# Optimization experiments

Hardware: AMD Instinct MI355X
Metric: run time of the kernel (lower is better)

Reference implementation:

```python
import jax, jax.numpy as jnp
import numpy as np

D = 768       # input_size
C = 8000      # num_classes
S = 4096      # seq_len
B = 2         # batch
SCALE = 1.0
LN_EPS = 1e-5


def setup_inputs() -> dict:
    key = jax.random.key(0)
    ks = jax.random.split(key, 8)
    std = 0.03  # module's _init_weights std
    return {
        "x": jax.random.normal(ks[0], (B, S, D), dtype=jnp.float32),
        "encoded_descriptions": jax.random.normal(ks[1], (C, D), dtype=jnp.float32),
        "Wk": jax.random.normal(ks[2], (D, D), dtype=jnp.float32) * std,
        "Wv": jax.random.normal(ks[3], (D, D), dtype=jnp.float32) * std,
        "bv": jax.random.normal(ks[4], (D,), dtype=jnp.float32) * 0.01,
        "ln_gamma": jnp.ones((D,), dtype=jnp.float32),
        "ln_beta": jnp.zeros((D,), dtype=jnp.float32),
        "out_w": jax.random.normal(ks[5], (D,), dtype=jnp.float32) * std,
        "out_b": jax.random.normal(ks[6], (), dtype=jnp.float32) * 0.01,
    }


def reference(x, encoded_descriptions, Wk, Wv, bv, ln_gamma, ln_beta, out_w, out_b):
    # V = x @ Wv^T + bv ; K = x @ Wk^T  (torch Linear applies weight transposed)
    V = jnp.einsum('bsd,ed->bse', x, Wv) + bv          # [B, S, D]
    K = jnp.einsum('bsd,ed->bse', x, Wk)               # [B, S, D]
    # att_weights = Q @ K^T, Q broadcast over batch -> [B, C, S]
    att = jnp.einsum('cd,bsd->bcs', encoded_descriptions, K)
    attention = jax.nn.softmax(att / SCALE, axis=2)    # [B, C, S]
    y = jnp.einsum('bcs,bsd->bcd', attention, V)       # [B, C, D]
    # LayerNorm over last dim
    mu = jnp.mean(y, axis=-1, keepdims=True)
    var = jnp.mean(jnp.square(y - mu), axis=-1, keepdims=True)
    y = (y - mu) * jax.lax.rsqrt(var + LN_EPS) * ln_gamma + ln_beta
    # output = sum over D of out_w * y + out_b  -> [B, C]
    out = jnp.einsum('bcd,d->bc', y, out_w) + out_b
    return out
```

## Files before the change

kernel.cpp:

```cpp
#include <hip/hip_runtime.h>


typedef _Float16 half8  __attribute__((ext_vector_type(8)));
typedef _Float16 half4v __attribute__((ext_vector_type(4)));
typedef float    f32x4  __attribute__((ext_vector_type(4)));
typedef float    f32x16 __attribute__((ext_vector_type(16)));

#define L2E 1.44269504088896340736f

__device__ __forceinline__ void gld_lds16(_Float16* lds, const _Float16* g) {
  __builtin_amdgcn_global_load_lds(
      (const __attribute__((address_space(1))) unsigned int*)g,
      (__attribute__((address_space(3))) unsigned int*)lds, 16, 0, 0);
}

__global__ void cvt_kernel(const float* __restrict__ src, _Float16* __restrict__ dst, int n4) {
  int i = blockIdx.x * blockDim.x + threadIdx.x;
  if (i >= n4) return;
  float4 v = reinterpret_cast<const float4*>(src)[i];
  half4v h; h[0] = (_Float16)v.x; h[1] = (_Float16)v.y; h[2] = (_Float16)v.z; h[3] = (_Float16)v.w;
  reinterpret_cast<half4v*>(dst)[i] = h;
}

template <int MODE>
__global__ __launch_bounds__(256, 2) void gemm_nt_f16(
    const _Float16* __restrict__ A, const _Float16* __restrict__ Bt,
    _Float16* __restrict__ C, const float* __restrict__ bias, int M, int N)
{
  __shared__ __align__(16) _Float16 As[2][128 * 64];
  __shared__ __align__(16) _Float16 Bs[2][128 * 64];
  const int tid = threadIdx.x;
  const int lane = tid & 63, wid = tid >> 6;
  const int ntn = N >> 7;
  const int mtile = blockIdx.x / ntn, ntile = blockIdx.x - mtile * ntn;
  const int m0 = mtile << 7, n0 = ntile << 7;
  const int wm = wid >> 1, wn = wid & 1;

  f32x4 acc[4][4] = {};

  auto stage = [&](int buf, int kt) {
#pragma unroll
    for (int j = 0; j < 4; ++j) {
      int idx = (j << 8) + tid;
      int row = idx >> 3, slot = idx & 7;
      int gc = (kt << 6) + ((slot ^ (row & 7)) << 3);
      _Float16* ldsbase_a = &As[buf][(size_t)(((j << 8) + (wid << 6)) << 3)];
      _Float16* ldsbase_b = &Bs[buf][(size_t)(((j << 8) + (wid << 6)) << 3)];
      gld_lds16(ldsbase_a, &A[(size_t)(m0 + row) * 768 + gc]);
      gld_lds16(ldsbase_b, &Bt[(size_t)(n0 + row) * 768 + gc]);
    }
  };

  stage(0, 0);
  __syncthreads();

  for (int kt = 0; kt < 12; ++kt) {
    int cur = kt & 1;
    if (kt < 11) stage(cur ^ 1, kt + 1);
#pragma unroll
    for (int ks = 0; ks < 2; ++ks) {
      half8 a[4], b[4];
      int dloc = (ks << 5) + ((lane >> 4) << 3);
#pragma unroll
      for (int mi = 0; mi < 4; ++mi) {
        int row = (wm << 6) + (mi << 4) + (lane & 15);
        a[mi] = *reinterpret_cast<const half8*>(&As[cur][row * 64 + (dloc ^ ((row & 7) << 3))]);
      }
#pragma unroll
      for (int ni = 0; ni < 4; ++ni) {
        int row = (wn << 6) + (ni << 4) + (lane & 15);
        b[ni] = *reinterpret_cast<const half8*>(&Bs[cur][row * 64 + (dloc ^ ((row & 7) << 3))]);
      }
#pragma unroll
      for (int mi = 0; mi < 4; ++mi)
#pragma unroll
        for (int ni = 0; ni < 4; ++ni)
          acc[mi][ni] = __builtin_amdgcn_mfma_f32_16x16x32_f16(a[mi], b[ni], acc[mi][ni], 0, 0, 0);
    }
    __syncthreads();
  }

#pragma unroll
  for (int mi = 0; mi < 4; ++mi)
#pragma unroll
    for (int ni = 0; ni < 4; ++ni) {
      int col = n0 + (wn << 6) + (ni << 4) + (lane & 15);
#pragma unroll
      for (int r = 0; r < 4; ++r) {
        int row = m0 + (wm << 6) + (mi << 4) + ((lane >> 4) << 2) + r;
        float v = acc[mi][ni][r];
        if (bias) v += bias[row];
        size_t a;
        if (MODE == 1) {
          a = ((size_t)(row >> 5) * 48 + (col >> 4)) * 512 + (row & 31) * 16 + (col & 15);
        } else {
          a = (((size_t)(col >> 12) * 24 + (row >> 5)) * 256 + ((col & 4095) >> 4)) * 512
              + (row & 31) * 16 + (col & 15);
        }
        C[a] = (_Float16)v;
      }
    }
}

#define QS_STRIDE 776
#define PS_STRIDE 264

__global__ __launch_bounds__(512, 2) void attn_kernel(
    const float* __restrict__ Qf, const _Float16* __restrict__ Kf,
    const _Float16* __restrict__ Vf,
    const float* __restrict__ gamma, const float* __restrict__ beta,
    const float* __restrict__ outw, const float* __restrict__ outb,
    float* __restrict__ out)
{
  __shared__ __align__(16) _Float16 Qs[64 * QS_STRIDE];
  __shared__ __align__(16) _Float16 Ps[64 * PS_STRIDE];
  __shared__ float redmax[8 * 64];
  __shared__ float redsum[8 * 64];
  __shared__ float gws[768];
  __shared__ float epi[64 * 25];
  __shared__ float lrowS[64];
  __shared__ float scal[2];

  const int tid = threadIdx.x;
  const int lane = tid & 63;
  const int wid = tid >> 6;
  const int l31 = lane & 31;
  const int lh = lane >> 5;

  int xcd = blockIdx.x & 7, i8 = blockIdx.x >> 3;
  int f = (xcd < 2) ? (xcd * 32 + i8) : (64 + (xcd - 2) * 31 + i8);
  const int bb = f / 125;
  const int ct = f - bb * 125;
  const int c0 = ct << 6;

  const int n0w = wid * 96;
  const int laneoff = l31 * 16 + lh * 8;
  const _Float16* kfb = Kf + ((size_t)(bb * 128 + wid) * 48) * 512 + laneoff;
  const _Float16* vfb = Vf + ((size_t)(bb * 24 + wid * 3) * 256) * 512 + laneoff;

  uint4 kp[8];
#pragma unroll
  for (int j = 0; j < 8; ++j) kp[j] = *reinterpret_cast<const uint4*>(kfb + j * 512);
  uint4 vp[4][3];
#pragma unroll
  for (int j = 0; j < 4; ++j) {
    vp[j][0] = *reinterpret_cast<const uint4*>(vfb + j * 512);
    vp[j][1] = *reinterpret_cast<const uint4*>(vfb + 131072 + j * 512);
    vp[j][2] = *reinterpret_cast<const uint4*>(vfb + 262144 + j * 512);
  }

#pragma unroll
  for (int i = 0; i < 24; ++i) {
    int idx = tid + (i << 9);
    int row = idx / 192, c4 = idx - row * 192;
    float4 v = reinterpret_cast<const float4*>(Qf)[(size_t)(c0 + row) * 192 + c4];
    half4v h; h[0] = (_Float16)v.x; h[1] = (_Float16)v.y; h[2] = (_Float16)v.z; h[3] = (_Float16)v.w;
    *reinterpret_cast<half4v*>(&Qs[row * QS_STRIDE + (c4 << 2)]) = h;
  }
  for (int i = tid; i < 768; i += 512) gws[i] = gamma[i] * outw[i];
  __syncthreads();
  if (tid < 64) {
    float g = 0.f, bw = 0.f;
#pragma unroll
    for (int j = 0; j < 12; ++j) { int d = tid + (j << 6); g += gws[d]; bw += beta[d] * outw[d]; }
#pragma unroll
    for (int m = 32; m; m >>= 1) { g += __shfl_xor(g, m); bw += __shfl_xor(bw, m); }
    if (tid == 0) { scal[0] = g; scal[1] = bw; }
  }

  float mrow0 = -1e30f, mrow1 = -1e30f, lrow0 = 0.f, lrow1 = 0.f;

  f32x16 acc00 = {}, acc01 = {}, acc02 = {};
  f32x16 acc10 = {}, acc11 = {}, acc12 = {};
  const _Float16* qrow0 = &Qs[l31 * QS_STRIDE + (lh << 3)];
  const _Float16* qrow1 = qrow0 + 32 * QS_STRIDE;

  for (int st = 0; st < 16; ++st) {
    const _Float16* kbc = kfb + (size_t)st * 196608;
    const _Float16* kbn = kbc + 196608;
    const _Float16* vb  = vfb + (size_t)st * 8192;
    const _Float16* vbn = vb + 8192;

    f32x16 qk0 = {}, qk1 = {};
#pragma unroll
    for (int k = 0; k < 48; ++k) {
      half8 kf = __builtin_bit_cast(half8, kp[k & 7]);
      if (k < 40)        kp[k & 7] = *reinterpret_cast<const uint4*>(kbc + (k + 8) * 512);
      else if (st < 15)  kp[k & 7] = *reinterpret_cast<const uint4*>(kbn + (k - 40) * 512);
      half8 qf0 = *reinterpret_cast<const half8*>(qrow0 + (k << 4));
      half8 qf1 = *reinterpret_cast<const half8*>(qrow1 + (k << 4));
      qk0 = __builtin_amdgcn_mfma_f32_32x32x16_f16(kf, qf0, qk0, 0, 0, 0);
      qk1 = __builtin_amdgcn_mfma_f32_32x32x16_f16(kf, qf1, qk1, 0, 0, 0);
    }

    float mx0 = qk0[0], mx1 = qk1[0];
#pragma unroll
    for (int r = 1; r < 16; ++r) { mx0 = fmaxf(mx0, qk0[r]); mx1 = fmaxf(mx1, qk1[r]); }
    mx0 = fmaxf(mx0, __shfl_xor(mx0, 32));
    mx1 = fmaxf(mx1, __shfl_xor(mx1, 32));
    if (lh == 0) {
      redmax[(wid << 6) + l31] = mx0;
      redmax[(wid << 6) + 32 + l31] = mx1;
    }
    __syncthreads();
    float pm0 = redmax[l31], pm1 = redmax[32 + l31];
#pragma unroll
    for (int w = 1; w < 8; ++w) {
      pm0 = fmaxf(pm0, redmax[(w << 6) + l31]);
      pm1 = fmaxf(pm1, redmax[(w << 6) + 32 + l31]);
    }
    float mn0 = fmaxf(mrow0, pm0), mn1 = fmaxf(mrow1, pm1);
    float rr0 = exp2f((mrow0 - mn0) * L2E), rr1 = exp2f((mrow1 - mn1) * L2E);
    mrow0 = mn0; mrow1 = mn1;

    float sum0 = 0.f, sum1 = 0.f;
    const int sb = (wid << 5) + (lh << 2);
#pragma unroll
    for (int q2 = 0; q2 < 4; ++q2) {
      float p0 = exp2f((qk0[4 * q2 + 0] - mn0) * L2E);
      float p1 = exp2f((qk0[4 * q2 + 1] - mn0) * L2E);
      float p2 = exp2f((qk0[4 * q2 + 2] - mn0) * L2E);
      float p3 = exp2f((qk0[4 * q2 + 3] - mn0) * L2E);
      sum0 += (p0 + p1) + (p2 + p3);
      half4v h; h[0] = (_Float16)p0; h[1] = (_Float16)p1; h[2] = (_Float16)p2; h[3] = (_Float16)p3;
      *reinterpret_cast<half4v*>(&Ps[l31 * PS_STRIDE + sb + (q2 << 3)]) = h;
      float u0 = exp2f((qk1[4 * q2 + 0] - mn1) * L2E);
      float u1 = exp2f((qk1[4 * q2 + 1] - mn1) * L2E);
      float u2 = exp2f((qk1[4 * q2 + 2] - mn1) * L2E);
      float u3 = exp2f((qk1[4 * q2 + 3] - mn1) * L2E);
      sum1 += (u0 + u1) + (u2 + u3);
      half4v h2; h2[0] = (_Float16)u0; h2[1] = (_Float16)u1; h2[2] = (_Float16)u2; h2[3] = (_Float16)u3;
      *reinterpret_cast<half4v*>(&Ps[(32 + l31) * PS_STRIDE + sb + (q2 << 3)]) = h2;
    }
    sum0 += __shfl_xor(sum0, 32);
    sum1 += __shfl_xor(sum1, 32);
    if (lh == 0) {
      redsum[(wid << 6) + l31] = sum0;
      redsum[(wid << 6) + 32 + l31] = sum1;
    }
    if (__any(rr0 < 1.0f) || __any(rr1 < 1.0f)) {
#pragma unroll
      for (int r = 0; r < 16; ++r) {
        int crow = (r & 3) + ((r >> 2) << 3) + (lh << 2);
        float rs0 = __shfl(rr0, crow);
        float rs1 = __shfl(rr1, crow);
        acc00[r] *= rs0; acc01[r] *= rs0; acc02[r] *= rs0;
        acc10[r] *= rs1; acc11[r] *= rs1; acc12[r] *= rs1;
      }
    }
    __syncthreads();
    {
      float s0 = redsum[l31], s1 = redsum[32 + l31];
#pragma unroll
      for (int w = 1; w < 8; ++w) {
        s0 += redsum[(w << 6) + l31];
        s1 += redsum[(w << 6) + 32 + l31];
      }
      lrow0 = lrow0 * rr0 + s0;
      lrow1 = lrow1 * rr1 + s1;
    }
#pragma unroll
    for (int ks = 0; ks < 16; ++ks) {
      half8 b0 = __builtin_bit_cast(half8, vp[ks & 3][0]);
      half8 b1 = __builtin_bit_cast(half8, vp[ks & 3][1]);
      half8 b2 = __builtin_bit_cast(half8, vp[ks & 3][2]);
      if (ks < 12) {
        vp[ks & 3][0] = *reinterpret_cast<const uint4*>(vb + (ks + 4) * 512);
        vp[ks & 3][1] = *reinterpret_cast<const uint4*>(vb + 131072 + (ks + 4) * 512);
        vp[ks & 3][2] = *reinterpret_cast<const uint4*>(vb + 262144 + (ks + 4) * 512);
      } else if (st < 15) {
        vp[ks & 3][0] = *reinterpret_cast<const uint4*>(vbn + (ks - 12) * 512);
        vp[ks & 3][1] = *reinterpret_cast<const uint4*>(vbn + 131072 + (ks - 12) * 512);
        vp[ks & 3][2] = *reinterpret_cast<const uint4*>(vbn + 262144 + (ks - 12) * 512);
      }
      half8 pa0 = *reinterpret_cast<const half8*>(&Ps[l31 * PS_STRIDE + (ks << 4) + (lh << 3)]);
      half8 pa1 = *reinterpret_cast<const half8*>(&Ps[(32 + l31) * PS_STRIDE + (ks << 4) + (lh << 3)]);
      acc00 = __builtin_amdgcn_mfma_f32_32x32x16_f16(pa0, b0, acc00, 0, 0, 0);
      acc01 = __builtin_amdgcn_mfma_f32_32x32x16_f16(pa0, b1, acc01, 0, 0, 0);
      acc02 = __builtin_amdgcn_mfma_f32_32x32x16_f16(pa0, b2, acc02, 0, 0, 0);
      acc10 = __builtin_amdgcn_mfma_f32_32x32x16_f16(pa1, b0, acc10, 0, 0, 0);
      acc11 = __builtin_amdgcn_mfma_f32_32x32x16_f16(pa1, b1, acc11, 0, 0, 0);
      acc12 = __builtin_amdgcn_mfma_f32_32x32x16_f16(pa1, b2, acc12, 0, 0, 0);
    }
  }

  if (wid == 0 && lh == 0) { lrowS[l31] = lrow0; lrowS[32 + l31] = lrow1; }
  float gw0 = gws[n0w + l31];
  float gw1 = gws[n0w + 32 + l31];
  float gw2 = gws[n0w + 64 + l31];
#pragma unroll
  for (int r = 0; r < 16; ++r) {
    int c = (r & 3) + ((r >> 2) << 3) + (lh << 2);
    {
      float y0 = acc00[r], y1 = acc01[r], y2 = acc02[r];
      float t1 = y0 + y1 + y2;
      float t2 = y0 * y0 + y1 * y1 + y2 * y2;
      float t3 = y0 * gw0 + y1 * gw1 + y2 * gw2;
#pragma unroll
      for (int m = 1; m <= 16; m <<= 1) {
        t1 += __shfl_xor(t1, m); t2 += __shfl_xor(t2, m); t3 += __shfl_xor(t3, m);
      }
      if (l31 == 0) { float* e = &epi[c * 25 + wid * 3]; e[0] = t1; e[1] = t2; e[2] = t3; }
    }
    {
      float y0 = acc10[r], y1 = acc11[r], y2 = acc12[r];
      float t1 = y0 + y1 + y2;
      float t2 = y0 * y0 + y1 * y1 + y2 * y2;
      float t3 = y0 * gw0 + y1 * gw1 + y2 * gw2;
#pragma unroll
      for (int m = 1; m <= 16; m <<= 1) {
        t1 += __shfl_xor(t1, m); t2 += __shfl_xor(t2, m); t3 += __shfl_xor(t3, m);
      }
      if (l31 == 0) { float* e = &epi[(32 + c) * 25 + wid * 3]; e[0] = t1; e[1] = t2; e[2] = t3; }
    }
  }
  __syncthreads();
  if (tid < 64) {
    float S1 = 0.f, S2 = 0.f, S3 = 0.f;
#pragma unroll
    for (int w = 0; w < 8; ++w) {
      const float* e = &epi[tid * 25 + w * 3];
      S1 += e[0]; S2 += e[1]; S3 += e[2];
    }
    float l = lrowS[tid];
    float invl = 1.0f / l;
    float mu = S1 * invl * (1.0f / 768.0f);
    float ey2 = S2 * invl * invl * (1.0f / 768.0f);
    float var = ey2 - mu * mu;
    float rs = rsqrtf(var + 1e-5f);
    float res = rs * (S3 * invl - mu * scal[0]) + scal[1] + outb[0];
    out[bb * 8000 + c0 + tid] = res;
  }
}

extern "C" void kernel_launch(void* const* d_in, const int* in_sizes, int n_in,
                              void* d_out, int out_size, void* d_ws, size_t ws_size,
                              hipStream_t stream) {
  (void)in_sizes; (void)n_in; (void)out_size; (void)ws_size;
  const float* x     = (const float*)d_in[0];
  const float* qenc  = (const float*)d_in[1];
  const float* Wk    = (const float*)d_in[2];
  const float* Wv    = (const float*)d_in[3];
  const float* bv    = (const float*)d_in[4];
  const float* gam   = (const float*)d_in[5];
  const float* bet   = (const float*)d_in[6];
  const float* outw  = (const float*)d_in[7];
  const float* outb  = (const float*)d_in[8];
  float* out = (float*)d_out;

  char* ws = (char*)d_ws;
  _Float16* x_h  = (_Float16*)(ws);
  _Float16* wk_h = (_Float16*)(ws + 12582912);
  _Float16* wv_h = (_Float16*)(ws + 13762560);
  _Float16* K_f  = (_Float16*)(ws + 14942208);
  _Float16* V_f  = (_Float16*)(ws + 27525120);

  cvt_kernel<<<6144, 256, 0, stream>>>(x, x_h, 1572864);
  cvt_kernel<<<576, 256, 0, stream>>>(Wk, wk_h, 147456);
  cvt_kernel<<<576, 256, 0, stream>>>(Wv, wv_h, 147456);
  gemm_nt_f16<1><<<384, 256, 0, stream>>>(x_h, wk_h, K_f, nullptr, 8192, 768);
  gemm_nt_f16<2><<<384, 256, 0, stream>>>(wv_h, x_h, V_f, bv, 768, 8192);
  attn_kernel<<<250, 512, 0, stream>>>(qenc, K_f, V_f, gam, bet, outw, outb, out);
}
```

Before: 392.6 us.

## Process two key tiles per softmax step with XOR-swizzled LDS and priority hints

The attention loop now handles 512 keys per iteration: QK^T runs on two K tiles per Q fragment, so row max/sum reductions and rescaling happen half as often. The second tile's probabilities are kept in registers and written to LDS after the first PV pass, with an extra barrier in between. The padded Q/P LDS strides are replaced by an XOR swizzle, Q fragments are software-prefetched one step ahead, and MFMA blocks are wrapped in s_setprio. Prefetch depth for K and V is reduced to save registers, which could expose more global-load latency.

```diff
diff --git a/kernel.cpp b/kernel.cpp
--- a/kernel.cpp
+++ b/kernel.cpp
@@ -102,9 +102,6 @@
     }
 }
 
-#define QS_STRIDE 776
-#define PS_STRIDE 264
-
 __global__ __launch_bounds__(512, 2) void attn_kernel(
     const float* __restrict__ Qf, const _Float16* __restrict__ Kf,
     const _Float16* __restrict__ Vf,
@@ -112,8 +109,8 @@
     const float* __restrict__ outw, const float* __restrict__ outb,
     float* __restrict__ out)
 {
-  __shared__ __align__(16) _Float16 Qs[64 * QS_STRIDE];
-  __shared__ __align__(16) _Float16 Ps[64 * PS_STRIDE];
+  __shared__ __align__(16) _Float16 Qs[64 * 768];
+  __shared__ __align__(16) _Float16 Ps[64 * 256];
   __shared__ float redmax[8 * 64];
   __shared__ float redsum[8 * 64];
   __shared__ float gws[768];
@@ -135,15 +132,19 @@
 
   const int n0w = wid * 96;
   const int laneoff = l31 * 16 + lh * 8;
+  const int qswz = (l31 & 15) << 3;
   const _Float16* kfb = Kf + ((size_t)(bb * 128 + wid) * 48) * 512 + laneoff;
   const _Float16* vfb = Vf + ((size_t)(bb * 24 + wid * 3) * 256) * 512 + laneoff;
 
-  uint4 kp[8];
-#pragma unroll
-  for (int j = 0; j < 8; ++j) kp[j] = *reinterpret_cast<const uint4*>(kfb + j * 512);
-  uint4 vp[4][3];
-#pragma unroll
-  for (int j = 0; j < 4; ++j) {
+  uint4 kpA[3], kpB[3];
+#pragma unroll
+  for (int j = 0; j < 3; ++j) {
+    kpA[j] = *reinterpret_cast<const uint4*>(kfb + j * 512);
+    kpB[j] = *reinterpret_cast<const uint4*>(kfb + 196608 + j * 512);
+  }
+  uint4 vp[2][3];
+#pragma unroll
+  for (int j = 0; j < 2; ++j) {
     vp[j][0] = *reinterpret_cast<const uint4*>(vfb + j * 512);
     vp[j][1] = *reinterpret_cast<const uint4*>(vfb + 131072 + j * 512);
     vp[j][2] = *reinterpret_cast<const uint4*>(vfb + 262144 + j * 512);
@@ -155,7 +156,7 @@
     int row = idx / 192, c4 = idx - row * 192;
     float4 v = reinterpret_cast<const float4*>(Qf)[(size_t)(c0 + row) * 192 + c4];
     half4v h; h[0] = (_Float16)v.x; h[1] = (_Float16)v.y; h[2] = (_Float16)v.z; h[3] = (_Float16)v.w;
-    *reinterpret_cast<half4v*>(&Qs[row * QS_STRIDE + (c4 << 2)]) = h;
+    *reinterpret_cast<half4v*>(&Qs[row * 768 + ((c4 << 2) ^ ((row & 15) << 3))]) = h;
   }
   for (int i = tid; i < 768; i += 512) gws[i] = gamma[i] * outw[i];
   __syncthreads();
@@ -172,30 +173,50 @@
 
   f32x16 acc00 = {}, acc01 = {}, acc02 = {};
   f32x16 acc10 = {}, acc11 = {}, acc12 = {};
-  const _Float16* qrow0 = &Qs[l31 * QS_STRIDE + (lh << 3)];
-  const _Float16* qrow1 = qrow0 + 32 * QS_STRIDE;
-
-  for (int st = 0; st < 16; ++st) {
-    const _Float16* kbc = kfb + (size_t)st * 196608;
-    const _Float16* kbn = kbc + 196608;
-    const _Float16* vb  = vfb + (size_t)st * 8192;
-    const _Float16* vbn = vb + 8192;
-
-    f32x16 qk0 = {}, qk1 = {};
+  const _Float16* qb0 = &Qs[l31 * 768];
+  const _Float16* qb1 = &Qs[(32 + l31) * 768];
+
+#pragma unroll 1
+  for (int st = 0; st < 8; ++st) {
+    const _Float16* kbA = kfb + (size_t)st * 393216;
+    const _Float16* kbB = kbA + 196608;
+    const _Float16* vtb = vfb + (size_t)st * 16384;
+    const bool more = (st < 7);
+
+    f32x16 qkA0 = {}, qkA1 = {}, qkB0 = {}, qkB1 = {};
+    half8 qc0 = *reinterpret_cast<const half8*>(qb0 + (((lh << 3)) ^ qswz));
+    half8 qc1 = *reinterpret_cast<const half8*>(qb1 + (((lh << 3)) ^ qswz));
 #pragma unroll
     for (int k = 0; k < 48; ++k) {
-      half8 kf = __builtin_bit_cast(half8, kp[k & 7]);
-      if (k < 40)        kp[k & 7] = *reinterpret_cast<const uint4*>(kbc + (k + 8) * 512);
-      else if (st < 15)  kp[k & 7] = *reinterpret_cast<const uint4*>(kbn + (k - 40) * 512);
-      half8 qf0 = *reinterpret_cast<const half8*>(qrow0 + (k << 4));
-      half8 qf1 = *reinterpret_cast<const half8*>(qrow1 + (k << 4));
-      qk0 = __builtin_amdgcn_mfma_f32_32x32x16_f16(kf, qf0, qk0, 0, 0, 0);
-      qk1 = __builtin_amdgcn_mfma_f32_32x32x16_f16(kf, qf1, qk1, 0, 0, 0);
-    }
-
-    float mx0 = qk0[0], mx1 = qk1[0];
-#pragma unroll
-    for (int r = 1; r < 16; ++r) { mx0 = fmaxf(mx0, qk0[r]); mx1 = fmaxf(mx1, qk1[r]); }
+      half8 kfAv = __builtin_bit_cast(half8, kpA[k % 3]);
+      half8 kfBv = __builtin_bit_cast(half8, kpB[k % 3]);
+      if (k < 45) {
+        kpA[k % 3] = *reinterpret_cast<const uint4*>(kbA + (k + 3) * 512);
+        kpB[k % 3] = *reinterpret_cast<const uint4*>(kbB + (k + 3) * 512);
+      } else if (more) {
+        kpA[k % 3] = *reinterpret_cast<const uint4*>(kbA + 393216 + (k - 45) * 512);
+        kpB[k % 3] = *reinterpret_cast<const uint4*>(kbB + 393216 + (k - 45) * 512);
+      }
+      half8 q0 = qc0, q1 = qc1;
+      if (k < 47) {
+        int col = (((k + 1) << 4) + (lh << 3)) ^ qswz;
+        qc0 = *reinterpret_cast<const half8*>(qb0 + col);
+        qc1 = *reinterpret_cast<const half8*>(qb1 + col);
+      }
+      __builtin_amdgcn_s_setprio(1);
+      qkA0 = __builtin_amdgcn_mfma_f32_32x32x16_f16(kfAv, q0, qkA0, 0, 0, 0);
+      qkA1 = __builtin_amdgcn_mfma_f32_32x32x16_f16(kfAv, q1, qkA1, 0, 0, 0);
+      qkB0 = __builtin_amdgcn_mfma_f32_32x32x16_f16(kfBv, q0, qkB0, 0, 0, 0);
+      qkB1 = __builtin_amdgcn_mfma_f32_32x32x16_f16(kfBv, q1, qkB1, 0, 0, 0);
+      __builtin_amdgcn_s_setprio(0);
+    }
+
+    float mx0 = fmaxf(qkA0[0], qkB0[0]), mx1 = fmaxf(qkA1[0], qkB1[0]);
+#pragma unroll
+    for (int r = 1; r < 16; ++r) {
+      mx0 = fmaxf(mx0, fmaxf(qkA0[r], qkB0[r]));
+      mx1 = fmaxf(mx1, fmaxf(qkA1[r], qkB1[r]));
+    }
     mx0 = fmaxf(mx0, __shfl_xor(mx0, 32));
     mx1 = fmaxf(mx1, __shfl_xor(mx1, 32));
     if (lh == 0) {
@@ -214,23 +235,38 @@
     mrow0 = mn0; mrow1 = mn1;
 
     float sum0 = 0.f, sum1 = 0.f;
-    const int sb = (wid << 5) + (lh << 2);
+    half4v pb0[4], pb1[4];
+    const int wcol = (wid << 5) + (lh << 2);
 #pragma unroll
     for (int q2 = 0; q2 < 4; ++q2) {
-      float p0 = exp2f((qk0[4 * q2 + 0] - mn0) * L2E);
-      float p1 = exp2f((qk0[4 * q2 + 1] - mn0) * L2E);
-      float p2 = exp2f((qk0[4 * q2 + 2] - mn0) * L2E);
-      float p3 = exp2f((qk0[4 * q2 + 3] - mn0) * L2E);
-      sum0 += (p0 + p1) + (p2 + p3);
-      half4v h; h[0] = (_Float16)p0; h[1] = (_Float16)p1; h[2] = (_Float16)p2; h[3] = (_Float16)p3;
-      *reinterpret_cast<half4v*>(&Ps[l31 * PS_STRIDE + sb + (q2 << 3)]) = h;
-      float u0 = exp2f((qk1[4 * q2 + 0] - mn1) * L2E);
-      float u1 = exp2f((qk1[4 * q2 + 1] - mn1) * L2E);
-      float u2 = exp2f((qk1[4 * q2 + 2] - mn1) * L2E);
-      float u3 = exp2f((qk1[4 * q2 + 3] - mn1) * L2E);
-      sum1 += (u0 + u1) + (u2 + u3);
-      half4v h2; h2[0] = (_Float16)u0; h2[1] = (_Float16)u1; h2[2] = (_Float16)u2; h2[3] = (_Float16)u3;
-      *reinterpret_cast<half4v*>(&Ps[(32 + l31) * PS_STRIDE + sb + (q2 << 3)]) = h2;
+      float a0 = exp2f((qkA0[4 * q2 + 0] - mn0) * L2E);
+      float a1 = exp2f((qkA0[4 * q2 + 1] - mn0) * L2E);
+      float a2 = exp2f((qkA0[4 * q2 + 2] - mn0) * L2E);
+      float a3 = exp2f((qkA0[4 * q2 + 3] - mn0) * L2E);
+      sum0 += (a0 + a1) + (a2 + a3);
+      half4v ha; ha[0] = (_Float16)a0; ha[1] = (_Float16)a1; ha[2] = (_Float16)a2; ha[3] = (_Float16)a3;
+      *reinterpret_cast<half4v*>(&Ps[(l31 << 8) + ((wcol + (q2 << 3)) ^ qswz)]) = ha;
+      float b0 = exp2f((qkA1[4 * q2 + 0] - mn1) * L2E);
+      float b1 = exp2f((qkA1[4 * q2 + 1] - mn1) * L2E);
+      float b2 = exp2f((qkA1[4 * q2 + 2] - mn1) * L2E);
+      float b3 = exp2f((qkA1[4 * q2 + 3] - mn1) * L2E);
+      sum1 += (b0 + b1) + (b2 + b3);
+      half4v hb; hb[0] = (_Float16)b0; hb[1] = (_Float16)b1; hb[2] = (_Float16)b2; hb[3] = (_Float16)b3;
+      *reinterpret_cast<half4v*>(&Ps[((32 + l31) << 8) + ((wcol + (q2 << 3)) ^ qswz)]) = hb;
+      float c0v = exp2f((qkB0[4 * q2 + 0] - mn0) * L2E);
+      float c1v = exp2f((qkB0[4 * q2 + 1] - mn0) * L2E);
+      float c2v = exp2f((qkB0[4 * q2 + 2] - mn0) * L2E);
+      float c3v = exp2f((qkB0[4 * q2 + 3] - mn0) * L2E);
+      sum0 += (c0v + c1v) + (c2v + c3v);
+      half4v hc; hc[0] = (_Float16)c0v; hc[1] = (_Float16)c1v; hc[2] = (_Float16)c2v; hc[3] = (_Float16)c3v;
+      pb0[q2] = hc;
+      float d0 = exp2f((qkB1[4 * q2 + 0] - mn1) * L2E);
+      float d1 = exp2f((qkB1[4 * q2 + 1] - mn1) * L2E);
+      float d2 = exp2f((qkB1[4 * q2 + 2] - mn1) * L2E);
+      float d3 = exp2f((qkB1[4 * q2 + 3] - mn1) * L2E);
+      sum1 += (d0 + d1) + (d2 + d3);
+      half4v hd; hd[0] = (_Float16)d0; hd[1] = (_Float16)d1; hd[2] = (_Float16)d2; hd[3] = (_Float16)d3;
+      pb1[q2] = hd;
     }
     sum0 += __shfl_xor(sum0, 32);
     sum1 += __shfl_xor(sum1, 32);
@@ -259,29 +295,46 @@
       lrow0 = lrow0 * rr0 + s0;
       lrow1 = lrow1 * rr1 + s1;
     }
-#pragma unroll
-    for (int ks = 0; ks < 16; ++ks) {
-      half8 b0 = __builtin_bit_cast(half8, vp[ks & 3][0]);
-      half8 b1 = __builtin_bit_cast(half8, vp[ks & 3][1]);
-      half8 b2 = __builtin_bit_cast(half8, vp[ks & 3][2]);
-      if (ks < 12) {
-        vp[ks & 3][0] = *reinterpret_cast<const uint4*>(vb + (ks + 4) * 512);
-        vp[ks & 3][1] = *reinterpret_cast<const uint4*>(vb + 131072 + (ks + 4) * 512);
-        vp[ks & 3][2] = *reinterpret_cast<const uint4*>(vb + 262144 + (ks + 4) * 512);
-      } else if (st < 15) {
-        vp[ks & 3][0] = *reinterpret_cast<const uint4*>(vbn + (ks - 12) * 512);
-        vp[ks & 3][1] = *reinterpret_cast<const uint4*>(vbn + 131072 + (ks - 12) * 512);
-        vp[ks & 3][2] = *reinterpret_cast<const uint4*>(vbn + 262144 + (ks - 12) * 512);
-      }
-      half8 pa0 = *reinterpret_cast<const half8*>(&Ps[l31 * PS_STRIDE + (ks << 4) + (lh << 3)]);
-      half8 pa1 = *reinterpret_cast<const half8*>(&Ps[(32 + l31) * PS_STRIDE + (ks << 4) + (lh << 3)]);
-      acc00 = __builtin_amdgcn_mfma_f32_32x32x16_f16(pa0, b0, acc00, 0, 0, 0);
-      acc01 = __builtin_amdgcn_mfma_f32_32x32x16_f16(pa0, b1, acc01, 0, 0, 0);
-      acc02 = __builtin_amdgcn_mfma_f32_32x32x16_f16(pa0, b2, acc02, 0, 0, 0);
-      acc10 = __builtin_amdgcn_mfma_f32_32x32x16_f16(pa1, b0, acc10, 0, 0, 0);
-      acc11 = __builtin_amdgcn_mfma_f32_32x32x16_f16(pa1, b1, acc11, 0, 0, 0);
-      acc12 = __builtin_amdgcn_mfma_f32_32x32x16_f16(pa1, b2, acc12, 0, 0, 0);
-    }
+
+#define PV_HALF(H)                                                             \
+    _Pragma("unroll")                                                          \
+    for (int ks = 0; ks < 16; ++ks) {                                          \
+      const int g = (H) * 16 + ks;                                             \
+      half8 b0 = __builtin_bit_cast(half8, vp[g & 1][0]);                      \
+      half8 b1 = __builtin_bit_cast(half8, vp[g & 1][1]);                      \
+      half8 b2 = __builtin_bit_cast(half8, vp[g & 1][2]);                      \
+      if (g < 30) {                                                            \
+        vp[g & 1][0] = *reinterpret_cast<const uint4*>(vtb + (g + 2) * 512);   \
+        vp[g & 1][1] = *reinterpret_cast<const uint4*>(vtb + 131072 + (g + 2) * 512); \
+        vp[g & 1][2] = *reinterpret_cast<const uint4*>(vtb + 262144 + (g + 2) * 512); \
+      } else if (more) {                                                       \
+        vp[g & 1][0] = *reinterpret_cast<const uint4*>(vtb + 16384 + (g - 30) * 512); \
+        vp[g & 1][1] = *reinterpret_cast<const uint4*>(vtb + 16384 + 131072 + (g - 30) * 512); \
+        vp[g & 1][2] = *reinterpret_cast<const uint4*>(vtb + 16384 + 262144 + (g - 30) * 512); \
+      }                                                                        \
+      int pcol = ((ks << 4) + (lh << 3)) ^ qswz;                               \
+      half8 pa0 = *reinterpret_cast<const half8*>(&Ps[(l31 << 8) + pcol]);     \
+      half8 pa1 = *reinterpret_cast<const half8*>(&Ps[((32 + l31) << 8) + pcol]); \
+      __builtin_amdgcn_s_setprio(1);                                           \
+      acc00 = __builtin_amdgcn_mfma_f32_32x32x16_f16(pa0, b0, acc00, 0, 0, 0); \
+      acc01 = __builtin_amdgcn_mfma_f32_32x32x16_f16(pa0, b1, acc01, 0, 0, 0); \
+      acc02 = __builtin_amdgcn_mfma_f32_32x32x16_f16(pa0, b2, acc02, 0, 0, 0); \
+      acc10 = __builtin_amdgcn_mfma_f32_32x32x16_f16(pa1, b0, acc10, 0, 0, 0); \
+      acc11 = __builtin_amdgcn_mfma_f32_32x32x16_f16(pa1, b1, acc11, 0, 0, 0); \
+      acc12 = __builtin_amdgcn_mfma_f32_32x32x16_f16(pa1, b2, acc12, 0, 0, 0); \
+      __builtin_amdgcn_s_setprio(0);                                           \
+    }
+
+    PV_HALF(0)
+    __syncthreads();
+#pragma unroll
+    for (int q2 = 0; q2 < 4; ++q2) {
+      *reinterpret_cast<half4v*>(&Ps[(l31 << 8) + ((wcol + (q2 << 3)) ^ qswz)]) = pb0[q2];
+      *reinterpret_cast<half4v*>(&Ps[((32 + l31) << 8) + ((wcol + (q2 << 3)) ^ qswz)]) = pb1[q2];
+    }
+    __syncthreads();
+    PV_HALF(1)
+#undef PV_HALF
   }
 
   if (wid == 0 && lh == 0) { lrowS[l31] = lrow0; lrowS[32 + l31] = lrow1; }
```

After: 1.011 ms. 157% more time.
